# Performance work log

Hardware: AMD Instinct MI355X
Metric: run time of the kernel (lower is better)

The kernel has to match this reference:

```python
import jax, jax.numpy as jnp
import numpy as np

B, E, V, L = 16384, 16, 1_000_000, 50
DENSE, ONEHOT, MULTIHOT = 13, 26, 2
UNITS = [64, 12]
NN_IN = E * (ONEHOT + MULTIHOT) + DENSE  # 16*28+13 = 461
CONCAT_IN = 1 + E + UNITS[-1]            # 29


def setup_inputs() -> dict:
    key = jax.random.key(0)
    ks = jax.random.split(key, 12)
    s = 0.02  # glorot-ish init scale
    return {
        "dense": jax.random.normal(ks[0], (B, DENSE), jnp.float32),
        "onehot": jax.random.randint(ks[1], (B, ONEHOT), 0, V, jnp.int32),
        "multihot_ids": jax.random.randint(ks[2], (B, MULTIHOT, L), 0, V, jnp.int32),
        "multihot_mask": jnp.ones((B, MULTIHOT, L), jnp.float32),
        "fm_w": jax.random.normal(ks[3], (V, 1), jnp.float32) * s,
        "fm_emb": jax.random.normal(ks[4], (V, E), jnp.float32) * s,
        "nn_w0": jax.random.normal(ks[5], (NN_IN, UNITS[0]), jnp.float32) * s,
        "nn_b0": jnp.zeros((UNITS[0],), jnp.float32),
        "nn_w1": jax.random.normal(ks[6], (UNITS[0], UNITS[1]), jnp.float32) * s,
        "nn_b1": jnp.zeros((UNITS[1],), jnp.float32),
        "concat_w": jax.random.normal(ks[7], (CONCAT_IN, 1), jnp.float32) * s,
        "concat_b": jnp.zeros((1,), jnp.float32),
    }


def reference(dense, onehot, multihot_ids, multihot_mask, fm_w, fm_emb,
              nn_w0, nn_b0, nn_w1, nn_b1, concat_w, concat_b):
    # --- embedding lookups ---
    onehot_emb = fm_emb[onehot]                      # [B, 26, E]
    mh_emb = fm_emb[multihot_ids]                    # [B, 2, L, E]
    m = multihot_mask[..., None]                     # [B, 2, L, 1]
    # embedding_lookup_sparse(combiner='mean') over valid slots; empty rows -> 0 (tf.pad)
    denom = jnp.maximum(jnp.sum(m, axis=2), 1.0)     # [B, 2, 1]
    multihot_emb = jnp.sum(mh_emb * m, axis=2) / denom  # [B, 2, E]
    cat_emb = jnp.concatenate([onehot_emb, multihot_emb], axis=1)  # [B, 28, E]

    # --- FM 1st order: sum_i w_i (x_i = 1) ---
    fm_1st = jnp.sum(fm_w[onehot], axis=1)           # [B, 1]

    # --- FM 2nd order (keep_k_dims=True): 0.5*((sum v)^2 - sum v^2) ---
    s = jnp.sum(cat_emb, axis=1)                     # [B, E]
    fm_2nd = 0.5 * (s * s - jnp.sum(cat_emb * cat_emb, axis=1))  # [B, E]

    # --- deep part ---
    nn_inp = jnp.concatenate([cat_emb.reshape(-1, E * (ONEHOT + MULTIHOT)), dense], axis=1)
    h = jax.nn.relu(nn_inp @ nn_w0 + nn_b0)
    h = jax.nn.relu(h @ nn_w1 + nn_b1)               # [B, 12]

    concat_inp = jnp.concatenate([fm_1st, fm_2nd, h], axis=1)  # [B, 29]
    return jax.nn.sigmoid(concat_inp @ concat_w + concat_b)    # [B, 1]
```

## Files before the change

### kernel.cpp

```cpp
#include <hip/hip_runtime.h>
#include <hip/hip_bf16.h>

#define BATCH 16384
#define EDIM  16
#define NOH   26
#define LL    50
#define KIN   461
#define KPAD  480

using bf16x8 = __attribute__((ext_vector_type(8))) short;
using f32x4  = __attribute__((ext_vector_type(4))) float;

static __device__ __forceinline__ unsigned short f2bf(float f) {
    union { float f; unsigned int u; } v; v.f = f;
    unsigned int r = v.u + 0x7FFFu + ((v.u >> 16) & 1u);
    return (unsigned short)(r >> 16);
}

__global__ __launch_bounds__(256) void ka(
    const float* __restrict__ dense,
    const int*   __restrict__ onehot,
    const int*   __restrict__ mh_ids,
    const float* __restrict__ mh_mask,
    const float* __restrict__ fm_w,
    const float* __restrict__ fm_emb,
    const float* __restrict__ concat_w,
    const float* __restrict__ concat_b,
    unsigned short* __restrict__ nn_inp,
    float* __restrict__ partial)
{
    const int wv = threadIdx.x >> 6;
    const int b  = (blockIdx.x << 2) + wv;
    const int l  = threadIdx.x & 63;
    const int s  = l >> 2;
    const int d  = l & 3;

    const float v1 = (s < 10) ? 1.f : 0.f;
    int oid0 = onehot[b * NOH + s];
    int oid1 = (s < 10) ? onehot[b * NOH + 16 + s] : 0;

    int   mid[7]; float mmk[7];
    #pragma unroll
    for (int p = 0; p < 7; ++p) {
        int pi = p * 16 + s;
        bool valid = pi < 100;
        int f = (pi >= 50) ? 1 : 0;
        int i = pi - f * 50;
        size_t off = ((size_t)b * 2 + f) * LL + i;
        mid[p] = valid ? mh_ids[off]  : 0;
        mmk[p] = valid ? mh_mask[off] : 0.f;
    }

    float4 e0 = *(const float4*)(fm_emb + (size_t)oid0 * EDIM + d * 4);
    float4 e1 = *(const float4*)(fm_emb + (size_t)oid1 * EDIM + d * 4);
    float  wsa = fm_w[oid0];
    float  wsb = fm_w[oid1];
    float4 gm[7];
    #pragma unroll
    for (int p = 0; p < 7; ++p)
        gm[p] = *(const float4*)(fm_emb + (size_t)mid[p] * EDIM + d * 4);

    e1.x *= v1; e1.y *= v1; e1.z *= v1; e1.w *= v1;
    float wsum = (d == 0) ? (wsa + v1 * wsb) : 0.f;

    unsigned short* row = nn_inp + (size_t)b * KPAD;
    {
        ushort4 u; u.x = f2bf(e0.x); u.y = f2bf(e0.y); u.z = f2bf(e0.z); u.w = f2bf(e0.w);
        *(ushort4*)(row + s * EDIM + d * 4) = u;
    }
    if (s < 10) {
        ushort4 u; u.x = f2bf(e1.x); u.y = f2bf(e1.y); u.z = f2bf(e1.z); u.w = f2bf(e1.w);
        *(ushort4*)(row + (16 + s) * EDIM + d * 4) = u;
    }

    float a0x=0,a0y=0,a0z=0,a0w=0, a1x=0,a1y=0,a1z=0,a1w=0, m0=0, m1=0;
    #pragma unroll
    for (int p = 0; p < 7; ++p) {
        int pi = p * 16 + s;
        float m = mmk[p];
        if (pi >= 50) { a1x += m*gm[p].x; a1y += m*gm[p].y; a1z += m*gm[p].z; a1w += m*gm[p].w; m1 += m; }
        else          { a0x += m*gm[p].x; a0y += m*gm[p].y; a0z += m*gm[p].z; a0w += m*gm[p].w; m0 += m; }
    }

    float ohx = e0.x + e1.x, ohy = e0.y + e1.y, ohz = e0.z + e1.z, ohw = e0.w + e1.w;
    float qx = e0.x*e0.x + e1.x*e1.x, qy = e0.y*e0.y + e1.y*e1.y;
    float qz = e0.z*e0.z + e1.z*e1.z, qw = e0.w*e0.w + e1.w*e1.w;

#define R4(v) { v += __shfl_xor(v, 4); v += __shfl_xor(v, 8); v += __shfl_xor(v, 16); v += __shfl_xor(v, 32); }
    R4(a0x) R4(a0y) R4(a0z) R4(a0w)
    R4(a1x) R4(a1y) R4(a1z) R4(a1w)
    R4(m0)  R4(m1)
    R4(ohx) R4(ohy) R4(ohz) R4(ohw)
    R4(qx)  R4(qy)  R4(qz)  R4(qw)
    R4(wsum)
#undef R4

    float inv0 = 1.f / fmaxf(m0, 1.f);
    float inv1 = 1.f / fmaxf(m1, 1.f);
    float h0x = a0x*inv0, h0y = a0y*inv0, h0z = a0z*inv0, h0w = a0w*inv0;
    float h1x = a1x*inv1, h1y = a1y*inv1, h1z = a1z*inv1, h1w = a1w*inv1;

    if (s == 0) {
        ushort4 u; u.x = f2bf(h0x); u.y = f2bf(h0y); u.z = f2bf(h0z); u.w = f2bf(h0w);
        *(ushort4*)(row + 26 * EDIM + d * 4) = u;
    }
    if (s == 1) {
        ushort4 u; u.x = f2bf(h1x); u.y = f2bf(h1y); u.z = f2bf(h1z); u.w = f2bf(h1w);
        *(ushort4*)(row + 27 * EDIM + d * 4) = u;
    }

    float sx = ohx + h0x + h1x, sy = ohy + h0y + h1y, sz = ohz + h0z + h1z, sw = ohw + h0w + h1w;
    float tx = qx + h0x*h0x + h1x*h1x, ty = qy + h0y*h0y + h1y*h1y;
    float tz = qz + h0z*h0z + h1z*h1z, tw = qw + h0w*h0w + h1w*h1w;
    float f2x = 0.5f * (sx*sx - tx), f2y = 0.5f * (sy*sy - ty);
    float f2z = 0.5f * (sz*sz - tz), f2w = 0.5f * (sw*sw - tw);

    float cw0 = concat_w[0];
    float c0 = concat_w[1 + d*4 + 0], c1 = concat_w[1 + d*4 + 1];
    float c2 = concat_w[1 + d*4 + 2], c3 = concat_w[1 + d*4 + 3];
    float part = f2x*c0 + f2y*c1 + f2z*c2 + f2w*c3 + wsum * cw0;
    part += __shfl_xor(part, 1);
    part += __shfl_xor(part, 2);
    if (l == 0) partial[b] = part + concat_b[0];

    if (l < 32) {
        float v = (l < 13) ? dense[b * 13 + l] : 0.f;
        row[448 + l] = f2bf(v);
    }
}

__global__ __launch_bounds__(256) void kb(
    const unsigned short* __restrict__ nn_inp,
    const float* __restrict__ w0,
    const float* __restrict__ b0,
    const float* __restrict__ w1,
    const float* __restrict__ b1,
    const float* __restrict__ concat_w,
    const float* __restrict__ partial,
    float* __restrict__ out)
{
    __shared__ unsigned short w0s[30720];
    __shared__ float w1t[12 * 64];
    __shared__ float b0s[64];
    __shared__ float b1s[12];
    __shared__ float cwh[12];
    __shared__ float h0s[4][16][68];

    const int t = threadIdx.x;

    for (int idx = t; idx < 30720; idx += 256) {
        int j    = idx & 7;
        int frag = idx >> 3;
        int lane = frag & 63;
        int tile = frag >> 6;
        int nt = tile / 15;
        int kt = tile - nt * 15;
        int k = kt * 32 + ((lane >> 4) << 3) + j;
        int n = (nt << 4) + (lane & 15);
        float v = (k < KIN) ? w0[k * 64 + n] : 0.f;
        w0s[idx] = f2bf(v);
    }
    for (int i = t; i < 768; i += 256) { int k = i / 12, j = i - k * 12; w1t[j * 64 + k] = w1[i]; }
    if (t < 64)  b0s[t] = b0[t];
    if (t >= 64 && t < 76)  b1s[t - 64] = b1[t - 64];
    if (t >= 96 && t < 108) cwh[t - 96] = concat_w[17 + (t - 96)];
    __syncthreads();

    const int wv = t >> 6, l = t & 63;
    const int row0 = (blockIdx.x << 6) + (wv << 4);
    const int c = l & 15, g = l >> 4;

    f32x4 acc0 = {0.f,0.f,0.f,0.f}, acc1 = acc0, acc2 = acc0, acc3 = acc0;
    const unsigned short* ap = nn_inp + (size_t)(row0 + c) * KPAD + (g << 3);
    const bf16x8* bp = (const bf16x8*)w0s + l;

    #pragma unroll
    for (int kt = 0; kt < 15; ++kt) {
        bf16x8 a = *(const bf16x8*)(ap + kt * 32);
        acc0 = __builtin_amdgcn_mfma_f32_16x16x32_bf16(a, bp[(0*15 + kt) * 64], acc0, 0, 0, 0);
        acc1 = __builtin_amdgcn_mfma_f32_16x16x32_bf16(a, bp[(1*15 + kt) * 64], acc1, 0, 0, 0);
        acc2 = __builtin_amdgcn_mfma_f32_16x16x32_bf16(a, bp[(2*15 + kt) * 64], acc2, 0, 0, 0);
        acc3 = __builtin_amdgcn_mfma_f32_16x16x32_bf16(a, bp[(3*15 + kt) * 64], acc3, 0, 0, 0);
    }

    #pragma unroll
    for (int reg = 0; reg < 4; ++reg) {
        int r = g * 4 + reg;
        h0s[wv][r][ 0 + c] = fmaxf(acc0[reg] + b0s[ 0 + c], 0.f);
        h0s[wv][r][16 + c] = fmaxf(acc1[reg] + b0s[16 + c], 0.f);
        h0s[wv][r][32 + c] = fmaxf(acc2[reg] + b0s[32 + c], 0.f);
        h0s[wv][r][48 + c] = fmaxf(acc3[reg] + b0s[48 + c], 0.f);
    }
    __syncthreads();

    float s0 = b1s[g*3 + 0], s1 = b1s[g*3 + 1], s2 = b1s[g*3 + 2];
    #pragma unroll
    for (int k4 = 0; k4 < 16; ++k4) {
        float4 h  = *(const float4*)&h0s[wv][c][k4 * 4];
        float4 wa = *(const float4*)&w1t[(g*3 + 0) * 64 + k4 * 4];
        float4 wb = *(const float4*)&w1t[(g*3 + 1) * 64 + k4 * 4];
        float4 wc = *(const float4*)&w1t[(g*3 + 2) * 64 + k4 * 4];
        s0 += h.x*wa.x + h.y*wa.y + h.z*wa.z + h.w*wa.w;
        s1 += h.x*wb.x + h.y*wb.y + h.z*wb.z + h.w*wb.w;
        s2 += h.x*wc.x + h.y*wc.y + h.z*wc.z + h.w*wc.w;
    }
    float hd = fmaxf(s0, 0.f)*cwh[g*3] + fmaxf(s1, 0.f)*cwh[g*3+1] + fmaxf(s2, 0.f)*cwh[g*3+2];
    hd += __shfl_xor(hd, 16);
    hd += __shfl_xor(hd, 32);
    if (g == 0) {
        int r = row0 + c;
        float x = partial[r] + hd;
        out[r] = 1.f / (1.f + __expf(-x));
    }
}

extern "C" void kernel_launch(void* const* d_in, const int* in_sizes, int n_in,
                              void* d_out, int out_size, void* d_ws, size_t ws_size,
                              hipStream_t stream) {
    const float* dense   = (const float*)d_in[0];
    const int*   onehot  = (const int*)  d_in[1];
    const int*   mh_ids  = (const int*)  d_in[2];
    const float* mh_mask = (const float*)d_in[3];
    const float* fm_w    = (const float*)d_in[4];
    const float* fm_emb  = (const float*)d_in[5];
    const float* w0      = (const float*)d_in[6];
    const float* b0      = (const float*)d_in[7];
    const float* w1      = (const float*)d_in[8];
    const float* b1      = (const float*)d_in[9];
    const float* cw      = (const float*)d_in[10];
    const float* cb      = (const float*)d_in[11];

    unsigned short* nn_inp = (unsigned short*)d_ws;
    float* partial = (float*)((char*)d_ws + (size_t)BATCH * KPAD * 2);
    float* out = (float*)d_out;

    hipLaunchKernelGGL(ka, dim3(BATCH / 4), dim3(256), 0, stream,
                       dense, onehot, mh_ids, mh_mask, fm_w, fm_emb, cw, cb, nn_inp, partial);
    hipLaunchKernelGGL(kb, dim3(BATCH / 64), dim3(256), 0, stream,
                       nn_inp, w0, b0, w1, b1, cw, partial, out);
}
```

Before: 192.2 us.

## Fuse embedding gather and MLP into one kernel staging activations in LDS

Merges the gather/FM kernel and the MLP kernel into a single 1024-thread kernel. Each 64-row block gathers embeddings straight into a padded LDS tile, replacing the bf16 nn_inp and partial workspace in global memory. The first-layer MFMA work is split so each of 16 waves computes one 16x16 output tile. This removes the global write and re-read of the intermediate plus a launch boundary. In exchange, each wave now processes four rows sequentially, and about 145 KB of LDS per block limits each CU to one block, which may reduce the memory parallelism available to hide random-gather latency.

After: 165.0 us. -14.2%, faster.

```diff
diff --git a/kernel.cpp b/kernel.cpp
--- a/kernel.cpp
+++ b/kernel.cpp
@@ -7,6 +7,7 @@
 #define LL    50
 #define KIN   461
 #define KPAD  480
+#define KLDS  488
 
 using bf16x8 = __attribute__((ext_vector_type(8))) short;
 using f32x4  = __attribute__((ext_vector_type(4))) float;
@@ -17,138 +18,38 @@
     return (unsigned short)(r >> 16);
 }
 
-__global__ __launch_bounds__(256) void ka(
+__global__ __launch_bounds__(1024) void fused(
     const float* __restrict__ dense,
     const int*   __restrict__ onehot,
     const int*   __restrict__ mh_ids,
     const float* __restrict__ mh_mask,
     const float* __restrict__ fm_w,
     const float* __restrict__ fm_emb,
-    const float* __restrict__ concat_w,
-    const float* __restrict__ concat_b,
-    unsigned short* __restrict__ nn_inp,
-    float* __restrict__ partial)
-{
-    const int wv = threadIdx.x >> 6;
-    const int b  = (blockIdx.x << 2) + wv;
-    const int l  = threadIdx.x & 63;
-    const int s  = l >> 2;
-    const int d  = l & 3;
-
-    const float v1 = (s < 10) ? 1.f : 0.f;
-    int oid0 = onehot[b * NOH + s];
-    int oid1 = (s < 10) ? onehot[b * NOH + 16 + s] : 0;
-
-    int   mid[7]; float mmk[7];
-    #pragma unroll
-    for (int p = 0; p < 7; ++p) {
-        int pi = p * 16 + s;
-        bool valid = pi < 100;
-        int f = (pi >= 50) ? 1 : 0;
-        int i = pi - f * 50;
-        size_t off = ((size_t)b * 2 + f) * LL + i;
-        mid[p] = valid ? mh_ids[off]  : 0;
-        mmk[p] = valid ? mh_mask[off] : 0.f;
-    }
-
-    float4 e0 = *(const float4*)(fm_emb + (size_t)oid0 * EDIM + d * 4);
-    float4 e1 = *(const float4*)(fm_emb + (size_t)oid1 * EDIM + d * 4);
-    float  wsa = fm_w[oid0];
-    float  wsb = fm_w[oid1];
-    float4 gm[7];
-    #pragma unroll
-    for (int p = 0; p < 7; ++p)
-        gm[p] = *(const float4*)(fm_emb + (size_t)mid[p] * EDIM + d * 4);
-
-    e1.x *= v1; e1.y *= v1; e1.z *= v1; e1.w *= v1;
-    float wsum = (d == 0) ? (wsa + v1 * wsb) : 0.f;
-
-    unsigned short* row = nn_inp + (size_t)b * KPAD;
-    {
-        ushort4 u; u.x = f2bf(e0.x); u.y = f2bf(e0.y); u.z = f2bf(e0.z); u.w = f2bf(e0.w);
-        *(ushort4*)(row + s * EDIM + d * 4) = u;
-    }
-    if (s < 10) {
-        ushort4 u; u.x = f2bf(e1.x); u.y = f2bf(e1.y); u.z = f2bf(e1.z); u.w = f2bf(e1.w);
-        *(ushort4*)(row + (16 + s) * EDIM + d * 4) = u;
-    }
-
-    float a0x=0,a0y=0,a0z=0,a0w=0, a1x=0,a1y=0,a1z=0,a1w=0, m0=0, m1=0;
-    #pragma unroll
-    for (int p = 0; p < 7; ++p) {
-        int pi = p * 16 + s;
-        float m = mmk[p];
-        if (pi >= 50) { a1x += m*gm[p].x; a1y += m*gm[p].y; a1z += m*gm[p].z; a1w += m*gm[p].w; m1 += m; }
-        else          { a0x += m*gm[p].x; a0y += m*gm[p].y; a0z += m*gm[p].z; a0w += m*gm[p].w; m0 += m; }
-    }
-
-    float ohx = e0.x + e1.x, ohy = e0.y + e1.y, ohz = e0.z + e1.z, ohw = e0.w + e1.w;
-    float qx = e0.x*e0.x + e1.x*e1.x, qy = e0.y*e0.y + e1.y*e1.y;
-    float qz = e0.z*e0.z + e1.z*e1.z, qw = e0.w*e0.w + e1.w*e1.w;
-
-#define R4(v) { v += __shfl_xor(v, 4); v += __shfl_xor(v, 8); v += __shfl_xor(v, 16); v += __shfl_xor(v, 32); }
-    R4(a0x) R4(a0y) R4(a0z) R4(a0w)
-    R4(a1x) R4(a1y) R4(a1z) R4(a1w)
-    R4(m0)  R4(m1)
-    R4(ohx) R4(ohy) R4(ohz) R4(ohw)
-    R4(qx)  R4(qy)  R4(qz)  R4(qw)
-    R4(wsum)
-#undef R4
-
-    float inv0 = 1.f / fmaxf(m0, 1.f);
-    float inv1 = 1.f / fmaxf(m1, 1.f);
-    float h0x = a0x*inv0, h0y = a0y*inv0, h0z = a0z*inv0, h0w = a0w*inv0;
-    float h1x = a1x*inv1, h1y = a1y*inv1, h1z = a1z*inv1, h1w = a1w*inv1;
-
-    if (s == 0) {
-        ushort4 u; u.x = f2bf(h0x); u.y = f2bf(h0y); u.z = f2bf(h0z); u.w = f2bf(h0w);
-        *(ushort4*)(row + 26 * EDIM + d * 4) = u;
-    }
-    if (s == 1) {
-        ushort4 u; u.x = f2bf(h1x); u.y = f2bf(h1y); u.z = f2bf(h1z); u.w = f2bf(h1w);
-        *(ushort4*)(row + 27 * EDIM + d * 4) = u;
-    }
-
-    float sx = ohx + h0x + h1x, sy = ohy + h0y + h1y, sz = ohz + h0z + h1z, sw = ohw + h0w + h1w;
-    float tx = qx + h0x*h0x + h1x*h1x, ty = qy + h0y*h0y + h1y*h1y;
-    float tz = qz + h0z*h0z + h1z*h1z, tw = qw + h0w*h0w + h1w*h1w;
-    float f2x = 0.5f * (sx*sx - tx), f2y = 0.5f * (sy*sy - ty);
-    float f2z = 0.5f * (sz*sz - tz), f2w = 0.5f * (sw*sw - tw);
-
-    float cw0 = concat_w[0];
-    float c0 = concat_w[1 + d*4 + 0], c1 = concat_w[1 + d*4 + 1];
-    float c2 = concat_w[1 + d*4 + 2], c3 = concat_w[1 + d*4 + 3];
-    float part = f2x*c0 + f2y*c1 + f2z*c2 + f2w*c3 + wsum * cw0;
-    part += __shfl_xor(part, 1);
-    part += __shfl_xor(part, 2);
-    if (l == 0) partial[b] = part + concat_b[0];
-
-    if (l < 32) {
-        float v = (l < 13) ? dense[b * 13 + l] : 0.f;
-        row[448 + l] = f2bf(v);
-    }
-}
-
-__global__ __launch_bounds__(256) void kb(
-    const unsigned short* __restrict__ nn_inp,
     const float* __restrict__ w0,
     const float* __restrict__ b0,
     const float* __restrict__ w1,
     const float* __restrict__ b1,
     const float* __restrict__ concat_w,
-    const float* __restrict__ partial,
+    const float* __restrict__ concat_b,
     float* __restrict__ out)
 {
+    __shared__ unsigned short As[64 * KLDS];
     __shared__ unsigned short w0s[30720];
+    __shared__ float h0s[64][68];
     __shared__ float w1t[12 * 64];
+    __shared__ float part_s[64];
     __shared__ float b0s[64];
     __shared__ float b1s[12];
     __shared__ float cwh[12];
-    __shared__ float h0s[4][16][68];
-
-    const int t = threadIdx.x;
-
-    for (int idx = t; idx < 30720; idx += 256) {
+
+    const int t  = threadIdx.x;
+    const int wv = t >> 6;
+    const int l  = t & 63;
+    const int s  = l >> 2;
+    const int d  = l & 3;
+    const int row0 = blockIdx.x << 6;
+
+    for (int idx = t; idx < 30720; idx += 1024) {
         int j    = idx & 7;
         int frag = idx >> 3;
         int lane = frag & 63;
@@ -160,57 +61,148 @@
         float v = (k < KIN) ? w0[k * 64 + n] : 0.f;
         w0s[idx] = f2bf(v);
     }
-    for (int i = t; i < 768; i += 256) { int k = i / 12, j = i - k * 12; w1t[j * 64 + k] = w1[i]; }
+    if (t < 768) { int k = t / 12, j = t - k * 12; w1t[j * 64 + k] = w1[t]; }
     if (t < 64)  b0s[t] = b0[t];
-    if (t >= 64 && t < 76)  b1s[t - 64] = b1[t - 64];
-    if (t >= 96 && t < 108) cwh[t - 96] = concat_w[17 + (t - 96)];
+    if (t >= 64 && t < 76)   b1s[t - 64] = b1[t - 64];
+    if (t >= 96 && t < 108)  cwh[t - 96] = concat_w[17 + (t - 96)];
+
+    for (int i = 0; i < 4; ++i) {
+        const int r = (wv << 2) + i;
+        const int b = row0 + r;
+
+        const float v1 = (s < 10) ? 1.f : 0.f;
+        int oid0 = onehot[b * NOH + s];
+        int oid1 = (s < 10) ? onehot[b * NOH + 16 + s] : 0;
+
+        int   mid[7]; float mmk[7];
+        #pragma unroll
+        for (int p = 0; p < 7; ++p) {
+            int pi = p * 16 + s;
+            bool valid = pi < 100;
+            int f = (pi >= 50) ? 1 : 0;
+            int ii = pi - f * 50;
+            size_t off = ((size_t)b * 2 + f) * LL + ii;
+            mid[p] = valid ? mh_ids[off]  : 0;
+            mmk[p] = valid ? mh_mask[off] : 0.f;
+        }
+
+        float4 e0 = *(const float4*)(fm_emb + (size_t)oid0 * EDIM + d * 4);
+        float4 e1 = *(const float4*)(fm_emb + (size_t)oid1 * EDIM + d * 4);
+        float  wsa = fm_w[oid0];
+        float  wsb = fm_w[oid1];
+        float4 gm[7];
+        #pragma unroll
+        for (int p = 0; p < 7; ++p)
+            gm[p] = *(const float4*)(fm_emb + (size_t)mid[p] * EDIM + d * 4);
+
+        e1.x *= v1; e1.y *= v1; e1.z *= v1; e1.w *= v1;
+        float wsum = (d == 0) ? (wsa + v1 * wsb) : 0.f;
+
+        unsigned short* rowp = As + r * KLDS;
+        {
+            ushort4 u; u.x = f2bf(e0.x); u.y = f2bf(e0.y); u.z = f2bf(e0.z); u.w = f2bf(e0.w);
+            *(ushort4*)(rowp + s * EDIM + d * 4) = u;
+        }
+        if (s < 10) {
+            ushort4 u; u.x = f2bf(e1.x); u.y = f2bf(e1.y); u.z = f2bf(e1.z); u.w = f2bf(e1.w);
+            *(ushort4*)(rowp + (16 + s) * EDIM + d * 4) = u;
+        }
+
+        float a0x=0,a0y=0,a0z=0,a0w=0, a1x=0,a1y=0,a1z=0,a1w=0, m0=0, m1=0;
+        #pragma unroll
+        for (int p = 0; p < 7; ++p) {
+            int pi = p * 16 + s;
+            float m = mmk[p];
+            if (pi >= 50) { a1x += m*gm[p].x; a1y += m*gm[p].y; a1z += m*gm[p].z; a1w += m*gm[p].w; m1 += m; }
+            else          { a0x += m*gm[p].x; a0y += m*gm[p].y; a0z += m*gm[p].z; a0w += m*gm[p].w; m0 += m; }
+        }
+
+        float ohx = e0.x + e1.x, ohy = e0.y + e1.y, ohz = e0.z + e1.z, ohw = e0.w + e1.w;
+        float qx = e0.x*e0.x + e1.x*e1.x, qy = e0.y*e0.y + e1.y*e1.y;
+        float qz = e0.z*e0.z + e1.z*e1.z, qw = e0.w*e0.w + e1.w*e1.w;
+
+#define R4(v) { v += __shfl_xor(v, 4); v += __shfl_xor(v, 8); v += __shfl_xor(v, 16); v += __shfl_xor(v, 32); }
+        R4(a0x) R4(a0y) R4(a0z) R4(a0w)
+        R4(a1x) R4(a1y) R4(a1z) R4(a1w)
+        R4(m0)  R4(m1)
+        R4(ohx) R4(ohy) R4(ohz) R4(ohw)
+        R4(qx)  R4(qy)  R4(qz)  R4(qw)
+        R4(wsum)
+#undef R4
+
+        float inv0 = 1.f / fmaxf(m0, 1.f);
+        float inv1 = 1.f / fmaxf(m1, 1.f);
+        float h0x = a0x*inv0, h0y = a0y*inv0, h0z = a0z*inv0, h0w = a0w*inv0;
+        float h1x = a1x*inv1, h1y = a1y*inv1, h1z = a1z*inv1, h1w = a1w*inv1;
+
+        if (s == 0) {
+            ushort4 u; u.x = f2bf(h0x); u.y = f2bf(h0y); u.z = f2bf(h0z); u.w = f2bf(h0w);
+            *(ushort4*)(rowp + 26 * EDIM + d * 4) = u;
+        }
+        if (s == 1) {
+            ushort4 u; u.x = f2bf(h1x); u.y = f2bf(h1y); u.z = f2bf(h1z); u.w = f2bf(h1w);
+            *(ushort4*)(rowp + 27 * EDIM + d * 4) = u;
+        }
+
+        float sx = ohx + h0x + h1x, sy = ohy + h0y + h1y, sz = ohz + h0z + h1z, sw = ohw + h0w + h1w;
+        float tx = qx + h0x*h0x + h1x*h1x, ty = qy + h0y*h0y + h1y*h1y;
+        float tz = qz + h0z*h0z + h1z*h1z, tw = qw + h0w*h0w + h1w*h1w;
+        float f2x = 0.5f * (sx*sx - tx), f2y = 0.5f * (sy*sy - ty);
+        float f2z = 0.5f * (sz*sz - tz), f2w = 0.5f * (sw*sw - tw);
+
+        float cw0 = concat_w[0];
+        float c0 = concat_w[1 + d*4 + 0], c1 = concat_w[1 + d*4 + 1];
+        float c2 = concat_w[1 + d*4 + 2], c3 = concat_w[1 + d*4 + 3];
+        float part = f2x*c0 + f2y*c1 + f2z*c2 + f2w*c3 + wsum * cw0;
+        part += __shfl_xor(part, 1);
+        part += __shfl_xor(part, 2);
+        if (l == 0) part_s[r] = part + concat_b[0];
+
+        if (l < 32) {
+            float v = (l < 13) ? dense[b * 13 + l] : 0.f;
+            rowp[448 + l] = f2bf(v);
+        }
+    }
     __syncthreads();
 
-    const int wv = t >> 6, l = t & 63;
-    const int row0 = (blockIdx.x << 6) + (wv << 4);
+    const int rt = wv >> 2, nt = wv & 3;
     const int c = l & 15, g = l >> 4;
 
-    f32x4 acc0 = {0.f,0.f,0.f,0.f}, acc1 = acc0, acc2 = acc0, acc3 = acc0;
-    const unsigned short* ap = nn_inp + (size_t)(row0 + c) * KPAD + (g << 3);
-    const bf16x8* bp = (const bf16x8*)w0s + l;
+    f32x4 acc = {0.f, 0.f, 0.f, 0.f};
+    const unsigned short* ap = As + (rt * 16 + c) * KLDS + (g << 3);
+    const bf16x8* bp = (const bf16x8*)w0s + nt * 15 * 64 + l;
 
     #pragma unroll
     for (int kt = 0; kt < 15; ++kt) {
         bf16x8 a = *(const bf16x8*)(ap + kt * 32);
-        acc0 = __builtin_amdgcn_mfma_f32_16x16x32_bf16(a, bp[(0*15 + kt) * 64], acc0, 0, 0, 0);
-        acc1 = __builtin_amdgcn_mfma_f32_16x16x32_bf16(a, bp[(1*15 + kt) * 64], acc1, 0, 0, 0);
-        acc2 = __builtin_amdgcn_mfma_f32_16x16x32_bf16(a, bp[(2*15 + kt) * 64], acc2, 0, 0, 0);
-        acc3 = __builtin_amdgcn_mfma_f32_16x16x32_bf16(a, bp[(3*15 + kt) * 64], acc3, 0, 0, 0);
+        acc = __builtin_amdgcn_mfma_f32_16x16x32_bf16(a, bp[kt * 64], acc, 0, 0, 0);
     }
 
     #pragma unroll
-    for (int reg = 0; reg < 4; ++reg) {
-        int r = g * 4 + reg;
-        h0s[wv][r][ 0 + c] = fmaxf(acc0[reg] + b0s[ 0 + c], 0.f);
-        h0s[wv][r][16 + c] = fmaxf(acc1[reg] + b0s[16 + c], 0.f);
-        h0s[wv][r][32 + c] = fmaxf(acc2[reg] + b0s[32 + c], 0.f);
-        h0s[wv][r][48 + c] = fmaxf(acc3[reg] + b0s[48 + c], 0.f);
-    }
+    for (int reg = 0; reg < 4; ++reg)
+        h0s[rt * 16 + g * 4 + reg][nt * 16 + c] = fmaxf(acc[reg] + b0s[nt * 16 + c], 0.f);
     __syncthreads();
 
-    float s0 = b1s[g*3 + 0], s1 = b1s[g*3 + 1], s2 = b1s[g*3 + 2];
-    #pragma unroll
-    for (int k4 = 0; k4 < 16; ++k4) {
-        float4 h  = *(const float4*)&h0s[wv][c][k4 * 4];
-        float4 wa = *(const float4*)&w1t[(g*3 + 0) * 64 + k4 * 4];
-        float4 wb = *(const float4*)&w1t[(g*3 + 1) * 64 + k4 * 4];
-        float4 wc = *(const float4*)&w1t[(g*3 + 2) * 64 + k4 * 4];
-        s0 += h.x*wa.x + h.y*wa.y + h.z*wa.z + h.w*wa.w;
-        s1 += h.x*wb.x + h.y*wb.y + h.z*wb.z + h.w*wb.w;
-        s2 += h.x*wc.x + h.y*wc.y + h.z*wc.z + h.w*wc.w;
-    }
-    float hd = fmaxf(s0, 0.f)*cwh[g*3] + fmaxf(s1, 0.f)*cwh[g*3+1] + fmaxf(s2, 0.f)*cwh[g*3+2];
-    hd += __shfl_xor(hd, 16);
-    hd += __shfl_xor(hd, 32);
-    if (g == 0) {
-        int r = row0 + c;
-        float x = partial[r] + hd;
-        out[r] = 1.f / (1.f + __expf(-x));
+    if (wv < 4) {
+        float s0 = b1s[g*3 + 0], s1 = b1s[g*3 + 1], s2 = b1s[g*3 + 2];
+        #pragma unroll
+        for (int k4 = 0; k4 < 16; ++k4) {
+            float4 h  = *(const float4*)&h0s[wv * 16 + c][k4 * 4];
+            float4 wa = *(const float4*)&w1t[(g*3 + 0) * 64 + k4 * 4];
+            float4 wb = *(const float4*)&w1t[(g*3 + 1) * 64 + k4 * 4];
+            float4 wc = *(const float4*)&w1t[(g*3 + 2) * 64 + k4 * 4];
+            s0 += h.x*wa.x + h.y*wa.y + h.z*wa.z + h.w*wa.w;
+            s1 += h.x*wb.x + h.y*wb.y + h.z*wb.z + h.w*wb.w;
+            s2 += h.x*wc.x + h.y*wc.y + h.z*wc.z + h.w*wc.w;
+        }
+        float hd = fmaxf(s0, 0.f)*cwh[g*3] + fmaxf(s1, 0.f)*cwh[g*3+1] + fmaxf(s2, 0.f)*cwh[g*3+2];
+        hd += __shfl_xor(hd, 16);
+        hd += __shfl_xor(hd, 32);
+        if (g == 0) {
+            int rr = row0 + wv * 16 + c;
+            float x = part_s[wv * 16 + c] + hd;
+            out[rr] = 1.f / (1.f + __expf(-x));
+        }
     }
 }
 
@@ -230,12 +222,7 @@
     const float* cw      = (const float*)d_in[10];
     const float* cb      = (const float*)d_in[11];
 
-    unsigned short* nn_inp = (unsigned short*)d_ws;
-    float* partial = (float*)((char*)d_ws + (size_t)BATCH * KPAD * 2);
-    float* out = (float*)d_out;
-
-    hipLaunchKernelGGL(ka, dim3(BATCH / 4), dim3(256), 0, stream,
-                       dense, onehot, mh_ids, mh_mask, fm_w, fm_emb, cw, cb, nn_inp, partial);
-    hipLaunchKernelGGL(kb, dim3(BATCH / 64), dim3(256), 0, stream,
-                       nn_inp, w0, b0, w1, b1, cw, partial, out);
+    hipLaunchKernelGGL(fused, dim3(BATCH / 64), dim3(1024), 0, stream,
+                       dense, onehot, mh_ids, mh_mask, fm_w, fm_emb,
+                       w0, b0, w1, b1, cw, cb, (float*)d_out);
 }
```
